# Optimization experiments

Hardware: AMD Instinct MI355X
Metric: run time of the kernel (lower is better)

The kernel has to match this reference:

```python
import jax, jax.numpy as jnp
import numpy as np

D, E, N, DD, K = 1024, 2048, 16, 64, 4  # d_model, d_inner, d_state, dt_rank, d_conv
B, L = 2, 1024
EPS = 1e-5


def setup_inputs() -> dict:
    key = jax.random.key(0)
    ks = jax.random.split(key, 12)
    f = lambda k, s, scale=0.02: (jax.random.normal(k, s, jnp.float32) * scale)
    return dict(
        resid=jax.random.normal(ks[0], (B, L, D), jnp.float32),
        workplace_h=jnp.zeros((B, E, N), jnp.float32),
        norm_w=jnp.ones((D,), jnp.float32),
        skip_w=f(ks[1], (E, D)),
        in_w=f(ks[2], (E, D)),
        conv_w=f(ks[3], (E, 1, K), 0.2),
        conv_b=jnp.zeros((E,), jnp.float32),
        wd1=f(ks[4], (DD, E)),
        wd2_w=f(ks[5], (E, DD)),
        wd2_b=jnp.zeros((E,), jnp.float32),
        wb=f(ks[6], (N, E)),
        wc=f(ks[7], (N, E)),
        A_log=f(ks[8], (E, N), 1.0),
        W_D=jnp.ones((E,), jnp.float32),
        out_w=f(ks[9], (D, E)),
    )


def reference(resid, workplace_h, norm_w, skip_w, in_w, conv_w, conv_b,
              wd1, wd2_w, wd2_b, wb, wc, A_log, W_D, out_w):
    # RMSNorm
    x = resid * jax.lax.rsqrt(jnp.mean(resid ** 2, -1, keepdims=True) + EPS) * norm_w
    skip = x @ skip_w.T                      # [B,L,E]
    xi = x @ in_w.T                          # [B,L,E]
    # depthwise causal conv1d (torch pads both sides then slices to L; equivalent to left-pad K-1)
    xc = jnp.swapaxes(xi, 1, 2)              # [B,E,L]
    xc = jax.lax.conv_general_dilated(
        xc, conv_w, window_strides=(1,), padding=[(K - 1, 0)],
        feature_group_count=E, dimension_numbers=('NCH', 'OIH', 'NCH'))
    xc = xc + conv_b[None, :, None]
    x2 = jax.nn.silu(jnp.swapaxes(xc, 1, 2))  # [B,L,E]

    A = -jnp.exp(A_log)                       # [E,N]
    delta = jax.nn.softplus((x2 @ wd1.T) @ wd2_w.T + wd2_b)   # [B,L,E]
    A_bar = jnp.exp(delta[..., None] * A)                      # [B,L,E,N]
    Bm = x2 @ wb.T                                             # [B,L,N]
    B_bar = delta[..., None] * Bm[:, :, None, :]               # [B,L,E,N]
    Cm = x2 @ wc.T                                             # [B,L,N]

    def step(h, inp):
        a, b_, xl, cl = inp                   # [B,E,N],[B,E,N],[B,E],[B,N]
        h = a * h + b_ * xl[..., None]
        y = jnp.einsum('ben,bn->be', h, cl)
        return h, y

    h0 = jnp.zeros_like(workplace_h)          # workplace_h is zeroed (h[:] = 0)
    xs = (jnp.swapaxes(A_bar, 0, 1), jnp.swapaxes(B_bar, 0, 1),
          jnp.swapaxes(x2, 0, 1), jnp.swapaxes(Cm, 0, 1))
    _, ys = jax.lax.scan(step, h0, xs)        # ys: [L,B,E]
    y = jnp.swapaxes(ys, 0, 1)                # [B,L,E]

    y = (y + x2 * W_D) * jax.nn.silu(skip)
    return resid + y @ out_w.T
```

## Files before the change

### kernel.cpp

```cpp
#include <hip/hip_runtime.h>
#include <math.h>

#define Dm 1024
#define Em 2048
#define Nm 16
#define DDm 64
#define Bb 2
#define Lm 1024
#define Mrows (Bb*Lm)
#define NCH 32
#define CLEN 32
#define KS 16
#define KSO 4
#define PREPB 26112

typedef __attribute__((ext_vector_type(8))) short bf16x8;
typedef __attribute__((ext_vector_type(4))) float f32x4;
typedef unsigned int u32;
typedef unsigned short u16;

__device__ __forceinline__ u16 f2bf(float f) {
    union { float f; u32 u; } v; v.f = f;
    u32 r = v.u + 0x7fffu + ((v.u >> 16) & 1u);
    return (u16)(r >> 16);
}
__device__ __forceinline__ float bf2f(u16 v) {
    union { u32 u; float f; } t; t.u = ((u32)v) << 16; return t.f;
}

__device__ __forceinline__ void async_copy16(const void* g, void* l) {
    __builtin_amdgcn_global_load_lds(
        (const __attribute__((address_space(1))) u32*)g,
        (__attribute__((address_space(3))) u32*)l,
        16, 0, 0);
}

__global__ __launch_bounds__(256) void prep_rms_kernel(const float* __restrict__ skip_w,
                                                       const float* __restrict__ in_w,
                                                       const float* __restrict__ out_w,
                                                       const float* __restrict__ wd2_w,
                                                       const float* __restrict__ wb,
                                                       const float* __restrict__ wc,
                                                       const float* __restrict__ wd1,
                                                       const float* __restrict__ resid,
                                                       const float* __restrict__ norm_w,
                                                       u16* __restrict__ skip_w_bf,
                                                       u16* __restrict__ in_w_bf,
                                                       u16* __restrict__ out_w_bf,
                                                       u16* __restrict__ wd2_bf,
                                                       u16* __restrict__ wtb,
                                                       u16* __restrict__ x) {
    if (blockIdx.x < PREPB) {
        const int R0 = 2097152, R1 = 4194304, R2 = 6291456, R3 = 6422528, R4 = 6684672;
        int i = blockIdx.x * 256 + threadIdx.x;
        if (i < R0) skip_w_bf[i] = f2bf(skip_w[i]);
        else if (i < R1) in_w_bf[i - R0] = f2bf(in_w[i - R0]);
        else if (i < R2) out_w_bf[i - R1] = f2bf(out_w[i - R1]);
        else if (i < R3) wd2_bf[i - R2] = f2bf(wd2_w[i - R2]);
        else if (i < R4) {
            int j = i - R3;
            int c = j >> 11, k = j & 2047;
            float v = 0.f;
            if (c < 16) v = wb[(size_t)c * Em + k];
            else if (c < 32) v = wc[(size_t)(c - 16) * Em + k];
            else if (c < 96) v = wd1[(size_t)(c - 32) * Em + k];
            wtb[j] = f2bf(v);
        }
        return;
    }
    int row = blockIdx.x - PREPB;
    const float* r = resid + (size_t)row * Dm;
    float s = 0.f;
    for (int i = threadIdx.x; i < Dm; i += 256) { float v = r[i]; s += v * v; }
    __shared__ float red[4];
    for (int off = 32; off; off >>= 1) s += __shfl_down(s, off, 64);
    if ((threadIdx.x & 63) == 0) red[threadIdx.x >> 6] = s;
    __syncthreads();
    if (threadIdx.x == 0) {
        float t = red[0] + red[1] + red[2] + red[3];
        red[0] = rsqrtf(t / (float)Dm + 1e-5f);
    }
    __syncthreads();
    float sc = red[0];
    u16* xo = x + (size_t)row * Dm;
    for (int i = threadIdx.x; i < Dm; i += 256) xo[i] = f2bf(r[i] * sc * norm_w[i]);
}


__global__ __launch_bounds__(256) void gemm_db(const u16* __restrict__ A,
                                               const u16* __restrict__ W,
                                               const float* __restrict__ bias,
                                               float* __restrict__ C,
                                               float* __restrict__ C2, int split,
                                               int M, int N, int lda, int klen, int act) {
    __shared__ __align__(16) u16 As[2][128 * 32];
    __shared__ __align__(16) u16 Ws[2][64 * 32];
    int tid = threadIdx.x;
    int lane = tid & 63, wave = tid >> 6;
    int bm = blockIdx.y * 128, bn = blockIdx.x * 64;
    int kbase = blockIdx.z * klen;
    int lm = lane & 15, lq = lane >> 4;
    int wm = (wave & 1) * 64, wn = (wave >> 1) * 32;

    f32x4 acc[4][2] = {};
    int ldrow = lane >> 2;
    int gchunk = ((lane & 3) ^ ((lane >> 3) & 3)) * 8;
    int rdoff = (lq ^ ((lm >> 1) & 3)) * 8;

    const u16* Arow0 = A + (size_t)(bm + wave * 16 + ldrow) * lda + gchunk;
    const u16* Arow1 = A + (size_t)(bm + 64 + wave * 16 + ldrow) * lda + gchunk;
    const u16* Wrow  = W + (size_t)(bn + wave * 16 + ldrow) * lda + gchunk;
    int ldsA = (wave * 16) * 32;
    int ldsA2 = (64 + wave * 16) * 32;

    int nIter = klen / 32;
    async_copy16(Arow0 + kbase, &As[0][ldsA]);
    async_copy16(Arow1 + kbase, &As[0][ldsA2]);
    async_copy16(Wrow + kbase, &Ws[0][ldsA]);
    __syncthreads();

    for (int it = 0; it < nIter; ++it) {
        int cur = it & 1, nxt = cur ^ 1;
        if (it + 1 < nIter) {
            int k0 = kbase + (it + 1) * 32;
            async_copy16(Arow0 + k0, &As[nxt][ldsA]);
            async_copy16(Arow1 + k0, &As[nxt][ldsA2]);
            async_copy16(Wrow + k0, &Ws[nxt][ldsA]);
        }
        bf16x8 a[4], b[2];
        #pragma unroll
        for (int mi = 0; mi < 4; ++mi)
            a[mi] = *(const bf16x8*)&As[cur][(wm + mi * 16 + lm) * 32 + rdoff];
        #pragma unroll
        for (int nj = 0; nj < 2; ++nj)
            b[nj] = *(const bf16x8*)&Ws[cur][(wn + nj * 16 + lm) * 32 + rdoff];
        #pragma unroll
        for (int mi = 0; mi < 4; ++mi)
            #pragma unroll
            for (int nj = 0; nj < 2; ++nj)
                acc[mi][nj] = __builtin_amdgcn_mfma_f32_16x16x32_bf16(a[mi], b[nj], acc[mi][nj], 0, 0, 0);
        __syncthreads();
    }

    int ldc = C2 ? split : N;
    size_t zoff = (size_t)blockIdx.z * M * ldc;
    #pragma unroll
    for (int nj = 0; nj < 2; ++nj) {
        int col = bn + wn + nj * 16 + lm;
        float bv = bias ? bias[col] : 0.f;
        float* Cp = C; int colw = col;
        if (C2 && col >= split) { Cp = C2; colw = col - split; }
        #pragma unroll
        for (int mi = 0; mi < 4; ++mi) {
            #pragma unroll
            for (int r = 0; r < 4; ++r) {
                int row = bm + wm + mi * 16 + lq * 4 + r;
                float v = acc[mi][nj][r] + bv;
                size_t off = zoff + (size_t)row * ldc + colw;
                if (act == 2) ((u16*)Cp)[off] = f2bf(v);
                else Cp[off] = v;
            }
        }
    }
}

__global__ __launch_bounds__(256) void gemm_smallk(const u16* __restrict__ A,
                                                   const u16* __restrict__ W,
                                                   const float* __restrict__ bias,
                                                   u16* __restrict__ C,
                                                   int M, int N, int lda, int klen, int act) {
    __shared__ __align__(16) u16 As[4][128 * 32];
    __shared__ __align__(16) u16 Ws[4][64 * 32];
    int tid = threadIdx.x;
    int lane = tid & 63, wave = tid >> 6;
    int bm = blockIdx.y * 128, bn = blockIdx.x * 64;
    int kbase = blockIdx.z * klen;
    int lm = lane & 15, lq = lane >> 4;
    int wm = (wave & 1) * 64, wn = (wave >> 1) * 32;

    f32x4 acc[4][2] = {};
    int ldrow = lane >> 2;
    int gchunk = ((lane & 3) ^ ((lane >> 3) & 3)) * 8;
    int rdoff = (lq ^ ((lm >> 1) & 3)) * 8;

    const u16* Arow0 = A + (size_t)(bm + wave * 16 + ldrow) * lda + gchunk;
    const u16* Arow1 = A + (size_t)(bm + 64 + wave * 16 + ldrow) * lda + gchunk;
    const u16* Wrow  = W + (size_t)(bn + wave * 16 + ldrow) * lda + gchunk;
    int ldsA = (wave * 16) * 32;
    int ldsA2 = (64 + wave * 16) * 32;

    int nIter = klen / 32;
    for (int it = 0; it < nIter; ++it) {
        int k0 = kbase + it * 32;
        async_copy16(Arow0 + k0, &As[it][ldsA]);
        async_copy16(Arow1 + k0, &As[it][ldsA2]);
        async_copy16(Wrow + k0, &Ws[it][ldsA]);
    }
    __syncthreads();

    for (int it = 0; it < nIter; ++it) {
        bf16x8 a[4], b[2];
        #pragma unroll
        for (int mi = 0; mi < 4; ++mi)
            a[mi] = *(const bf16x8*)&As[it][(wm + mi * 16 + lm) * 32 + rdoff];
        #pragma unroll
        for (int nj = 0; nj < 2; ++nj)
            b[nj] = *(const bf16x8*)&Ws[it][(wn + nj * 16 + lm) * 32 + rdoff];
        #pragma unroll
        for (int mi = 0; mi < 4; ++mi)
            #pragma unroll
            for (int nj = 0; nj < 2; ++nj)
                acc[mi][nj] = __builtin_amdgcn_mfma_f32_16x16x32_bf16(a[mi], b[nj], acc[mi][nj], 0, 0, 0);
    }

    size_t zoff = (size_t)blockIdx.z * M * N;
    #pragma unroll
    for (int nj = 0; nj < 2; ++nj) {
        int col = bn + wn + nj * 16 + lm;
        float bv = bias ? bias[col] : 0.f;
        #pragma unroll
        for (int mi = 0; mi < 4; ++mi) {
            #pragma unroll
            for (int r = 0; r < 4; ++r) {
                int row = bm + wm + mi * 16 + lq * 4 + r;
                float v = acc[mi][nj][r] + bv;
                if (act == 1)
                    v = fmaxf(v, 0.f) + __logf(1.f + __expf(-fabsf(v)));
                C[zoff + (size_t)row * N + col] = f2bf(v);
            }
        }
    }
}

__global__ __launch_bounds__(256) void out_reduce_kernel(const u16* __restrict__ part,
                                                         const float* __restrict__ resid,
                                                         float* __restrict__ out) {
    int idx = blockIdx.x * 256 + threadIdx.x;
    float4 s = ((const float4*)resid)[idx];
    const int planeQ = Mrows * Dm / 4;
    #pragma unroll
    for (int ks = 0; ks < KSO; ++ks) {
        ushort4 p = ((const ushort4*)part)[(size_t)ks * planeQ + idx];
        s.x += bf2f(p.x); s.y += bf2f(p.y); s.z += bf2f(p.z); s.w += bf2f(p.w);
    }
    ((float4*)out)[idx] = s;
}

__global__ __launch_bounds__(256) void small_reduce_kernel(const u16* __restrict__ Cp,
                                                           float* __restrict__ Bm,
                                                           float* __restrict__ Cm,
                                                           u16* __restrict__ d1) {
    int idx = blockIdx.x * 256 + threadIdx.x;
    int row = idx >> 7, col = idx & 127;
    float s = 0.f;
    #pragma unroll
    for (int ks = 0; ks < KS; ++ks) s += bf2f(Cp[(size_t)ks * (Mrows * 128) + idx]);
    if (col < 16) Bm[(size_t)row * 16 + col] = s;
    else if (col < 32) Cm[(size_t)row * 16 + (col - 16)] = s;
    else if (col < 96) d1[(size_t)row * 64 + (col - 32)] = f2bf(s);
}

__global__ __launch_bounds__(256) void conv_silu_kernel(const u16* __restrict__ xi,
                                                        const float* __restrict__ cw,
                                                        const float* __restrict__ cb,
                                                        u16* __restrict__ x2b, int total) {
    int idx = blockIdx.x * 256 + threadIdx.x;
    if (idx >= total) return;
    int e = idx & (Em - 1);
    int l = (idx >> 11) & (Lm - 1);
    const u16* base = xi + idx;
    float w0 = cw[e * 4 + 0], w1 = cw[e * 4 + 1], w2 = cw[e * 4 + 2], w3 = cw[e * 4 + 3];
    float acc = cb[e];
    if (l >= 3) acc += w0 * bf2f(base[-3 * Em]);
    if (l >= 2) acc += w1 * bf2f(base[-2 * Em]);
    if (l >= 1) acc += w2 * bf2f(base[-1 * Em]);
    acc += w3 * bf2f(base[0]);
    float v = acc / (1.f + __expf(-acc));
    x2b[idx] = f2bf(v);
}

__global__ __launch_bounds__(256) void scan1_kernel(const u16* __restrict__ delta,
                                                    const u16* __restrict__ x2b,
                                                    const float* __restrict__ Bm,
                                                    const float* __restrict__ A_log,
                                                    float* __restrict__ h_end,
                                                    float* __restrict__ P) {
    int e = (blockIdx.x & 7) * 256 + threadIdx.x;
    int bc = blockIdx.x >> 3;
    int b = bc & 1, c = bc >> 1;
    float A[16];
    {
        const float4* al = (const float4*)(A_log + e * 16);
        float4 q0 = al[0], q1 = al[1], q2 = al[2], q3 = al[3];
        A[0]=-expf(q0.x); A[1]=-expf(q0.y); A[2]=-expf(q0.z); A[3]=-expf(q0.w);
        A[4]=-expf(q1.x); A[5]=-expf(q1.y); A[6]=-expf(q1.z); A[7]=-expf(q1.w);
        A[8]=-expf(q2.x); A[9]=-expf(q2.y); A[10]=-expf(q2.z); A[11]=-expf(q2.w);
        A[12]=-expf(q3.x); A[13]=-expf(q3.y); A[14]=-expf(q3.z); A[15]=-expf(q3.w);
    }
    float h[16], Pr[16];
    #pragma unroll
    for (int k = 0; k < 16; ++k) { h[k] = 0.f; Pr[k] = 1.f; }

    int l0 = c * CLEN;
    const u16* dp  = delta + ((size_t)(b * Lm + l0)) * Em + e;
    const u16* xp  = x2b   + ((size_t)(b * Lm + l0)) * Em + e;
    const float* bp = Bm   + ((size_t)(b * Lm + l0)) * Nm;

    float d_n = bf2f(dp[0]), x_n = bf2f(xp[0]);
    float4 b0n = *(const float4*)(bp + 0), b1n = *(const float4*)(bp + 4);
    float4 b2n = *(const float4*)(bp + 8), b3n = *(const float4*)(bp + 12);

    #pragma unroll 1
    for (int l = 0; l < CLEN; ++l) {
        float d = d_n, xv = x_n;
        float4 b0 = b0n, b1 = b1n, b2 = b2n, b3 = b3n;
        if (l < CLEN - 1) {
            d_n = bf2f(dp[(size_t)(l + 1) * Em]); x_n = bf2f(xp[(size_t)(l + 1) * Em]);
            const float* nb = bp + (size_t)(l + 1) * Nm;
            b0n = *(const float4*)(nb); b1n = *(const float4*)(nb + 4);
            b2n = *(const float4*)(nb + 8); b3n = *(const float4*)(nb + 12);
        }
        float dx = d * xv;
        float bb[16] = {b0.x,b0.y,b0.z,b0.w, b1.x,b1.y,b1.z,b1.w,
                        b2.x,b2.y,b2.z,b2.w, b3.x,b3.y,b3.z,b3.w};
        #pragma unroll
        for (int k = 0; k < 16; ++k) {
            float a = __expf(d * A[k]);
            h[k] = a * h[k] + bb[k] * dx;
            Pr[k] *= a;
        }
    }
    size_t base = (((size_t)c * 2 + b) * 16) * 2048 + e;
    #pragma unroll
    for (int k = 0; k < 16; ++k) {
        h_end[base + k * 2048] = h[k];
        P[base + k * 2048] = Pr[k];
    }
}

__global__ __launch_bounds__(256) void scan2_kernel(float* __restrict__ h_end,
                                                    const float* __restrict__ P) {
    int T = blockIdx.x * 256 + threadIdx.x;
    float hi = 0.f;
    float he_n = h_end[T], p_n = P[T];
    #pragma unroll 1
    for (int c = 0; c < NCH; ++c) {
        float he = he_n, p = p_n;
        if (c < NCH - 1) {
            he_n = h_end[(size_t)(c + 1) * 65536 + T];
            p_n  = P[(size_t)(c + 1) * 65536 + T];
        }
        float hnew = fmaf(p, hi, he);
        h_end[(size_t)c * 65536 + T] = hi;
        hi = hnew;
    }
}

__global__ __launch_bounds__(256) void scan3_kernel(const u16* __restrict__ delta,
                                                    const u16* __restrict__ x2b,
                                                    const float* __restrict__ Bm,
                                                    const float* __restrict__ Cm,
                                                    const float* __restrict__ A_log,
                                                    const float* __restrict__ h_init,
                                                    const u16* __restrict__ skip,
                                                    const float* __restrict__ W_D,
                                                    u16* __restrict__ yb) {
    int e = (blockIdx.x & 7) * 256 + threadIdx.x;
    int bc = blockIdx.x >> 3;
    int b = bc & 1, c = bc >> 1;
    float A[16];
    {
        const float4* al = (const float4*)(A_log + e * 16);
        float4 q0 = al[0], q1 = al[1], q2 = al[2], q3 = al[3];
        A[0]=-expf(q0.x); A[1]=-expf(q0.y); A[2]=-expf(q0.z); A[3]=-expf(q0.w);
        A[4]=-expf(q1.x); A[5]=-expf(q1.y); A[6]=-expf(q1.z); A[7]=-expf(q1.w);
        A[8]=-expf(q2.x); A[9]=-expf(q2.y); A[10]=-expf(q2.z); A[11]=-expf(q2.w);
        A[12]=-expf(q3.x); A[13]=-expf(q3.y); A[14]=-expf(q3.z); A[15]=-expf(q3.w);
    }
    float h[16];
    {
        size_t base = (((size_t)c * 2 + b) * 16) * 2048 + e;
        #pragma unroll
        for (int k = 0; k < 16; ++k) h[k] = h_init[base + k * 2048];
    }
    float wd = W_D[e];

    int l0 = c * CLEN;
    const u16* dp  = delta + ((size_t)(b * Lm + l0)) * Em + e;
    const u16* xp  = x2b   + ((size_t)(b * Lm + l0)) * Em + e;
    const u16* sp  = skip  + ((size_t)(b * Lm + l0)) * Em + e;
    const float* bp = Bm   + ((size_t)(b * Lm + l0)) * Nm;
    const float* cp = Cm   + ((size_t)(b * Lm + l0)) * Nm;
    u16* yp = yb + ((size_t)(b * Lm + l0)) * Em + e;

    float d_n = bf2f(dp[0]), x_n = bf2f(xp[0]), s_n = bf2f(sp[0]);
    float4 b0n = *(const float4*)(bp + 0), b1n = *(const float4*)(bp + 4);
    float4 b2n = *(const float4*)(bp + 8), b3n = *(const float4*)(bp + 12);
    float4 c0n = *(const float4*)(cp + 0), c1n = *(const float4*)(cp + 4);
    float4 c2n = *(const float4*)(cp + 8), c3n = *(const float4*)(cp + 12);

    #pragma unroll 1
    for (int l = 0; l < CLEN; ++l) {
        float d = d_n, xv = x_n, sv = s_n;
        float4 b0 = b0n, b1 = b1n, b2 = b2n, b3 = b3n;
        float4 c0 = c0n, c1 = c1n, c2 = c2n, c3 = c3n;
        if (l < CLEN - 1) {
            d_n = bf2f(dp[(size_t)(l + 1) * Em]); x_n = bf2f(xp[(size_t)(l + 1) * Em]);
            s_n = bf2f(sp[(size_t)(l + 1) * Em]);
            const float* nb = bp + (size_t)(l + 1) * Nm;
            b0n = *(const float4*)(nb); b1n = *(const float4*)(nb + 4);
            b2n = *(const float4*)(nb + 8); b3n = *(const float4*)(nb + 12);
            const float* nc = cp + (size_t)(l + 1) * Nm;
            c0n = *(const float4*)(nc); c1n = *(const float4*)(nc + 4);
            c2n = *(const float4*)(nc + 8); c3n = *(const float4*)(nc + 12);
        }
        float dx = d * xv;
        float bb[16] = {b0.x,b0.y,b0.z,b0.w, b1.x,b1.y,b1.z,b1.w,
                        b2.x,b2.y,b2.z,b2.w, b3.x,b3.y,b3.z,b3.w};
        float cc[16] = {c0.x,c0.y,c0.z,c0.w, c1.x,c1.y,c1.z,c1.w,
                        c2.x,c2.y,c2.z,c2.w, c3.x,c3.y,c3.z,c3.w};
        float yv = 0.f;
        #pragma unroll
        for (int k = 0; k < 16; ++k) {
            float a = __expf(d * A[k]);
            h[k] = a * h[k] + bb[k] * dx;
            yv += h[k] * cc[k];
        }
        float sig = 1.f / (1.f + __expf(-sv));
        yp[(size_t)l * Em] = f2bf((yv + xv * wd) * (sv * sig));
    }
}

extern "C" void kernel_launch(void* const* d_in, const int* in_sizes, int n_in,
                              void* d_out, int out_size, void* d_ws, size_t ws_size,
                              hipStream_t stream) {
    const float* resid  = (const float*)d_in[0];
    const float* norm_w = (const float*)d_in[2];
    const float* skip_w = (const float*)d_in[3];
    const float* in_w   = (const float*)d_in[4];
    const float* conv_w = (const float*)d_in[5];
    const float* conv_b = (const float*)d_in[6];
    const float* wd1    = (const float*)d_in[7];
    const float* wd2_w  = (const float*)d_in[8];
    const float* wd2_b  = (const float*)d_in[9];
    const float* wb     = (const float*)d_in[10];
    const float* wc     = (const float*)d_in[11];
    const float* A_log  = (const float*)d_in[12];
    const float* W_D    = (const float*)d_in[13];
    const float* out_w  = (const float*)d_in[14];
    float* out = (float*)d_out;

    float* ws = (float*)d_ws;
    float* region0 = ws; ws += 3 * 1024 * 1024;
    u16* x_bf      = (u16*)region0;
    u16* skip_w_bf = (u16*)(region0 + 1024 * 1024);
    u16* in_w_bf   = (u16*)(region0 + 2 * 1024 * 1024);
    float* h_endb  = region0;
    u16* out_w_bf  = (u16*)ws; ws += 1024 * 1024;
    u16* wd2_bf    = (u16*)ws; ws += 65536;
    u16* d1_bf     = (u16*)ws; ws += 65536;
    u16* wtb       = (u16*)ws; ws += 131072;
    float* Pbuf    = ws; ws += 2 * 1024 * 1024;
    u16* Cpart16   = (u16*)ws; ws += (size_t)KS * Mrows * 128 / 2;
    u16* skip_bf   = (u16*)ws; ws += (size_t)Mrows * Em / 2;
    u16* xi_bf     = (u16*)ws; ws += (size_t)Mrows * Em / 2;
    u16* x2_bf     = (u16*)ws; ws += (size_t)Mrows * Em / 2;
    u16* yb_bf     = (u16*)ws; ws += (size_t)Mrows * Em / 2;
    u16* OutPart16 = (u16*)ws; ws += (size_t)KSO * Mrows * Dm / 2;
    float* Bmb     = ws; ws += (size_t)Mrows * Nm;
    float* Cmb     = ws; ws += (size_t)Mrows * Nm;
    u16* delta16   = xi_bf;

    const int M = Mrows;

    prep_rms_kernel<<<PREPB + M, 256, 0, stream>>>(
        skip_w, in_w, out_w, wd2_w, wb, wc, wd1, resid, norm_w,
        skip_w_bf, in_w_bf, out_w_bf, wd2_bf, wtb, x_bf);

    gemm_db<<<dim3(2 * Em / 64, M / 128, 1), 256, 0, stream>>>(
        x_bf, skip_w_bf, nullptr, (float*)skip_bf, (float*)xi_bf, Em, M, 2 * Em, Dm, Dm, 2);

    conv_silu_kernel<<<(M * Em) / 256, 256, 0, stream>>>(xi_bf, conv_w, conv_b, x2_bf, M * Em);

    gemm_smallk<<<dim3(128 / 64, M / 128, KS), 256, 0, stream>>>(
        x2_bf, wtb, nullptr, Cpart16, M, 128, Em, Em / KS, 0);
    small_reduce_kernel<<<(M * 128) / 256, 256, 0, stream>>>(Cpart16, Bmb, Cmb, d1_bf);

    gemm_smallk<<<dim3(Em / 64, M / 128, 1), 256, 0, stream>>>(
        d1_bf, wd2_bf, wd2_b, delta16, M, Em, DDm, DDm, 1);

    scan1_kernel<<<Bb * NCH * 8, 256, 0, stream>>>(delta16, x2_bf, Bmb, A_log, h_endb, Pbuf);
    scan2_kernel<<<65536 / 256, 256, 0, stream>>>(h_endb, Pbuf);
    scan3_kernel<<<Bb * NCH * 8, 256, 0, stream>>>(delta16, x2_bf, Bmb, Cmb, A_log, h_endb,
                                                   skip_bf, W_D, yb_bf);

    gemm_db<<<dim3(Dm / 64, M / 128, KSO), 256, 0, stream>>>(
        yb_bf, out_w_bf, nullptr, (float*)OutPart16, nullptr, 0, M, Dm, Em, Em / KSO, 2);
    out_reduce_kernel<<<(M * Dm / 4) / 256, 256, 0, stream>>>(OutPart16, resid, out);
}
```

Before: 261.2 us.

## Double the scan chunk count and prefetch two steps ahead in scan kernels

Splits the sequence into 64 chunks of 16 steps instead of 32 chunks of 32, doubling the parallel blocks in the chunked selective scan. Both scan kernels now keep a two-deep register ring of prefetched delta/x/B/C values, loading step l+2 while step l is computed, to hide global load latency. The h_end and P buffers double in size and move out of the aliased region into their own workspace. The trade-off is a longer sequential cross-chunk combine pass, more carry-state traffic and higher register pressure.

```diff
diff --git a/kernel.cpp b/kernel.cpp
--- a/kernel.cpp
+++ b/kernel.cpp
@@ -8,8 +8,8 @@
 #define Bb 2
 #define Lm 1024
 #define Mrows (Bb*Lm)
-#define NCH 32
-#define CLEN 32
+#define NCH 64
+#define CLEN 16
 #define KS 16
 #define KSO 4
 #define PREPB 26112
@@ -306,21 +306,31 @@
     const u16* xp  = x2b   + ((size_t)(b * Lm + l0)) * Em + e;
     const float* bp = Bm   + ((size_t)(b * Lm + l0)) * Nm;
 
-    float d_n = bf2f(dp[0]), x_n = bf2f(xp[0]);
-    float4 b0n = *(const float4*)(bp + 0), b1n = *(const float4*)(bp + 4);
-    float4 b2n = *(const float4*)(bp + 8), b3n = *(const float4*)(bp + 12);
+    float dv[2], xv[2];
+    float4 bq[2][4];
+    #pragma unroll
+    for (int s = 0; s < 2; ++s) {
+        dv[s] = bf2f(dp[(size_t)s * Em]);
+        xv[s] = bf2f(xp[(size_t)s * Em]);
+        const float* nb = bp + (size_t)s * Nm;
+        bq[s][0] = *(const float4*)(nb); bq[s][1] = *(const float4*)(nb + 4);
+        bq[s][2] = *(const float4*)(nb + 8); bq[s][3] = *(const float4*)(nb + 12);
+    }
 
     #pragma unroll 1
     for (int l = 0; l < CLEN; ++l) {
-        float d = d_n, xv = x_n;
-        float4 b0 = b0n, b1 = b1n, b2 = b2n, b3 = b3n;
-        if (l < CLEN - 1) {
-            d_n = bf2f(dp[(size_t)(l + 1) * Em]); x_n = bf2f(xp[(size_t)(l + 1) * Em]);
-            const float* nb = bp + (size_t)(l + 1) * Nm;
-            b0n = *(const float4*)(nb); b1n = *(const float4*)(nb + 4);
-            b2n = *(const float4*)(nb + 8); b3n = *(const float4*)(nb + 12);
-        }
-        float dx = d * xv;
+        int cur = l & 1;
+        float d = dv[cur], xvv = xv[cur];
+        float4 b0 = bq[cur][0], b1 = bq[cur][1], b2 = bq[cur][2], b3 = bq[cur][3];
+        if (l + 2 < CLEN) {
+            size_t lo = (size_t)(l + 2);
+            dv[cur] = bf2f(dp[lo * Em]);
+            xv[cur] = bf2f(xp[lo * Em]);
+            const float* nb = bp + lo * Nm;
+            bq[cur][0] = *(const float4*)(nb); bq[cur][1] = *(const float4*)(nb + 4);
+            bq[cur][2] = *(const float4*)(nb + 8); bq[cur][3] = *(const float4*)(nb + 12);
+        }
+        float dx = d * xvv;
         float bb[16] = {b0.x,b0.y,b0.z,b0.w, b1.x,b1.y,b1.z,b1.w,
                         b2.x,b2.y,b2.z,b2.w, b3.x,b3.y,b3.z,b3.w};
         #pragma unroll
@@ -393,28 +403,40 @@
     const float* cp = Cm   + ((size_t)(b * Lm + l0)) * Nm;
     u16* yp = yb + ((size_t)(b * Lm + l0)) * Em + e;
 
-    float d_n = bf2f(dp[0]), x_n = bf2f(xp[0]), s_n = bf2f(sp[0]);
-    float4 b0n = *(const float4*)(bp + 0), b1n = *(const float4*)(bp + 4);
-    float4 b2n = *(const float4*)(bp + 8), b3n = *(const float4*)(bp + 12);
-    float4 c0n = *(const float4*)(cp + 0), c1n = *(const float4*)(cp + 4);
-    float4 c2n = *(const float4*)(cp + 8), c3n = *(const float4*)(cp + 12);
+    float dv[2], xv[2], sv2[2];
+    float4 bq[2][4], cq[2][4];
+    #pragma unroll
+    for (int s = 0; s < 2; ++s) {
+        dv[s] = bf2f(dp[(size_t)s * Em]);
+        xv[s] = bf2f(xp[(size_t)s * Em]);
+        sv2[s] = bf2f(sp[(size_t)s * Em]);
+        const float* nb = bp + (size_t)s * Nm;
+        bq[s][0] = *(const float4*)(nb); bq[s][1] = *(const float4*)(nb + 4);
+        bq[s][2] = *(const float4*)(nb + 8); bq[s][3] = *(const float4*)(nb + 12);
+        const float* nc = cp + (size_t)s * Nm;
+        cq[s][0] = *(const float4*)(nc); cq[s][1] = *(const float4*)(nc + 4);
+        cq[s][2] = *(const float4*)(nc + 8); cq[s][3] = *(const float4*)(nc + 12);
+    }
 
     #pragma unroll 1
     for (int l = 0; l < CLEN; ++l) {
-        float d = d_n, xv = x_n, sv = s_n;
-        float4 b0 = b0n, b1 = b1n, b2 = b2n, b3 = b3n;
-        float4 c0 = c0n, c1 = c1n, c2 = c2n, c3 = c3n;
-        if (l < CLEN - 1) {
-            d_n = bf2f(dp[(size_t)(l + 1) * Em]); x_n = bf2f(xp[(size_t)(l + 1) * Em]);
-            s_n = bf2f(sp[(size_t)(l + 1) * Em]);
-            const float* nb = bp + (size_t)(l + 1) * Nm;
-            b0n = *(const float4*)(nb); b1n = *(const float4*)(nb + 4);
-            b2n = *(const float4*)(nb + 8); b3n = *(const float4*)(nb + 12);
-            const float* nc = cp + (size_t)(l + 1) * Nm;
-            c0n = *(const float4*)(nc); c1n = *(const float4*)(nc + 4);
-            c2n = *(const float4*)(nc + 8); c3n = *(const float4*)(nc + 12);
-        }
-        float dx = d * xv;
+        int cur = l & 1;
+        float d = dv[cur], xvv = xv[cur], sv = sv2[cur];
+        float4 b0 = bq[cur][0], b1 = bq[cur][1], b2 = bq[cur][2], b3 = bq[cur][3];
+        float4 c0 = cq[cur][0], c1 = cq[cur][1], c2 = cq[cur][2], c3 = cq[cur][3];
+        if (l + 2 < CLEN) {
+            size_t lo = (size_t)(l + 2);
+            dv[cur] = bf2f(dp[lo * Em]);
+            xv[cur] = bf2f(xp[lo * Em]);
+            sv2[cur] = bf2f(sp[lo * Em]);
+            const float* nb = bp + lo * Nm;
+            bq[cur][0] = *(const float4*)(nb); bq[cur][1] = *(const float4*)(nb + 4);
+            bq[cur][2] = *(const float4*)(nb + 8); bq[cur][3] = *(const float4*)(nb + 12);
+            const float* nc = cp + lo * Nm;
+            cq[cur][0] = *(const float4*)(nc); cq[cur][1] = *(const float4*)(nc + 4);
+            cq[cur][2] = *(const float4*)(nc + 8); cq[cur][3] = *(const float4*)(nc + 12);
+        }
+        float dx = d * xvv;
         float bb[16] = {b0.x,b0.y,b0.z,b0.w, b1.x,b1.y,b1.z,b1.w,
                         b2.x,b2.y,b2.z,b2.w, b3.x,b3.y,b3.z,b3.w};
         float cc[16] = {c0.x,c0.y,c0.z,c0.w, c1.x,c1.y,c1.z,c1.w,
@@ -427,7 +449,7 @@
             yv += h[k] * cc[k];
         }
         float sig = 1.f / (1.f + __expf(-sv));
-        yp[(size_t)l * Em] = f2bf((yv + xv * wd) * (sv * sig));
+        yp[(size_t)l * Em] = f2bf((yv + xvv * wd) * (sv * sig));
     }
 }
 
@@ -455,12 +477,12 @@
     u16* x_bf      = (u16*)region0;
     u16* skip_w_bf = (u16*)(region0 + 1024 * 1024);
     u16* in_w_bf   = (u16*)(region0 + 2 * 1024 * 1024);
-    float* h_endb  = region0;
     u16* out_w_bf  = (u16*)ws; ws += 1024 * 1024;
     u16* wd2_bf    = (u16*)ws; ws += 65536;
     u16* d1_bf     = (u16*)ws; ws += 65536;
     u16* wtb       = (u16*)ws; ws += 131072;
-    float* Pbuf    = ws; ws += 2 * 1024 * 1024;
+    float* h_endb  = ws; ws += 4 * 1024 * 1024;
+    float* Pbuf    = ws; ws += 4 * 1024 * 1024;
     u16* Cpart16   = (u16*)ws; ws += (size_t)KS * Mrows * 128 / 2;
     u16* skip_bf   = (u16*)ws; ws += (size_t)Mrows * Em / 2;
     u16* xi_bf     = (u16*)ws; ws += (size_t)Mrows * Em / 2;
```

Result: slower. 434.5 us (+66.4%).
